# Optimization experiments

Hardware: AMD Instinct MI355X
Metric: run time of the kernel (lower is better)

Reference implementation:

```python
import jax, jax.numpy as jnp
import numpy as np

B, C, VC, H, W = 4, 256, 128, 64, 64


def setup_inputs() -> dict:
    key = jax.random.key(0)
    kx, kq, kk, kv = jax.random.split(key, 4)
    # Conv2d 1x1 no-bias weights are just [out_channels, in_channels] matrices.
    s = 1.0 / np.sqrt(C)
    return {
        "x": jax.random.normal(kx, (B, C, H, W), dtype=jnp.float32),
        "Wq": jax.random.uniform(kq, (VC, C), minval=-s, maxval=s, dtype=jnp.float32),
        "Wk": jax.random.uniform(kk, (VC, C), minval=-s, maxval=s, dtype=jnp.float32),
        "Wv": jax.random.uniform(kv, (VC, C), minval=-s, maxval=s, dtype=jnp.float32),
    }


def reference(x, Wq, Wk, Wv):
    # 1x1 convs == per-pixel channel GEMMs
    Q = jnp.einsum('bchw,dc->bdhw', x, Wq)  # [B, VC, H, W]
    K = jnp.einsum('bchw,dc->bdhw', x, Wk)
    V = jnp.einsum('bchw,dc->bdhw', x, Wv)
    b, d, h, w = Q.shape
    # affinity over all spatial pairs: [B, H, W, H, W]
    aff = jnp.einsum('bdij,bdkl->bijkl', Q, K).reshape(b, h, w, h * w)
    aff = jax.nn.softmax(aff, axis=3).reshape(b, h, w, h, w)
    # attention-weighted aggregation of values
    out = jnp.einsum('bijkl,bdkl->bdij', aff, V)  # [B, VC, H, W]
    return out
```

## Files before the change

### kernel.cpp

```cpp
#include <hip/hip_runtime.h>
#include <hip/hip_bf16.h>

#define B_ 4
#define C_ 256
#define D_ 128
#define N_ 4096

typedef float f32x4 __attribute__((ext_vector_type(4)));
typedef short bf16x8 __attribute__((ext_vector_type(8)));
typedef short s16x4 __attribute__((ext_vector_type(4)));
typedef unsigned short u16;
typedef unsigned int u32;

__device__ __forceinline__ u16 f2bf(float f) {
  unsigned u = __float_as_uint(f);
  u += 0x7fffu + ((u >> 16) & 1u);
  return (u16)(u >> 16);
}
__device__ __forceinline__ float bf2f(u16 v) {
  return __uint_as_float(((u32)v) << 16);
}
__device__ __forceinline__ u32 cvt_pk_bf16(float a, float b) {
  u32 r;
  asm("v_cvt_pk_bf16_f32 %0, %1, %2" : "=v"(r) : "v"(a), "v"(b));
  return r;
}

__global__ __launch_bounds__(256) void castw_kernel(
    const float* __restrict__ Wq, const float* __restrict__ Wk,
    const float* __restrict__ Wv, u16* __restrict__ Whi,
    u16* __restrict__ Wlo) {
  const int i = blockIdx.x * 256 + threadIdx.x;
  const int m = i >> 13;
  const int j = (i & 8191) * 4;
  const float* src = (m == 0) ? Wq : (m == 1) ? Wk : Wv;
  const float scale = (m == 0) ? 1.44269504f : 1.0f;
  const float4 v = *(const float4*)(src + j);
  const float vv[4] = {v.x * scale, v.y * scale, v.z * scale, v.w * scale};
  s16x4 h, l;
#pragma unroll
  for (int k = 0; k < 4; ++k) {
    const u16 hb = f2bf(vv[k]);
    h[k] = (short)hb;
    l[k] = (short)f2bf(vv[k] - bf2f(hb));
  }
  *(s16x4*)&Whi[m * 32768 + j] = h;
  *(s16x4*)&Wlo[m * 32768 + j] = l;
}

__global__ __launch_bounds__(256, 2) void proj_kernel(
    const float* __restrict__ x, const u16* __restrict__ Whi,
    const u16* __restrict__ Wlo, u16* __restrict__ Qo, u16* __restrict__ Ko,
    u16* __restrict__ Vt) {
  __shared__ __align__(16) u16 xs_h[32 * 256];
  __shared__ __align__(16) u16 xs_l[32 * 256];

  const int n0 = blockIdx.x * 32;
  const int b = blockIdx.y;
  const int t = threadIdx.x;
  const int w = t >> 6, lane = t & 63, g = lane >> 4, c = lane & 15;

  {
    const float* xb = x + ((size_t)b * C_) * N_ + n0;
#pragma unroll
    for (int r = 0; r < 8; ++r) {
      const int id = r * 256 + t;
      const int cr = id >> 3, nq = (id & 7) * 4;
      const float4 v = *(const float4*)(xb + (size_t)cr * N_ + nq);
      const float vv[4] = {v.x, v.y, v.z, v.w};
#pragma unroll
      for (int k2 = 0; k2 < 4; ++k2) {
        const int idx2 = (nq + k2) * 256 + (cr ^ (((nq + k2) & 7) << 3));
        const u16 hb = f2bf(vv[k2]);
        xs_h[idx2] = hb;
        xs_l[idx2] = f2bf(vv[k2] - bf2f(hb));
      }
    }
  }
  __syncthreads();

  if (w < 2) {
    const size_t wo = (size_t)w * 32768;
    u16* __restrict__ O = (w == 0 ? Qo : Ko) + (size_t)b * N_ * D_;
#pragma unroll 1
    for (int dt = 0; dt < 8; ++dt) {
      bf16x8 wfh[8], wfl[8];
#pragma unroll
      for (int kc = 0; kc < 8; ++kc) {
        const size_t off = wo + (size_t)(dt * 16 + c) * 256 + kc * 32 + g * 8;
        wfh[kc] = *(const bf16x8*)&Whi[off];
        wfl[kc] = *(const bf16x8*)&Wlo[off];
      }
#pragma unroll
      for (int nt = 0; nt < 2; ++nt) {
        f32x4 a = {0.f, 0.f, 0.f, 0.f};
#pragma unroll
        for (int kc = 0; kc < 8; ++kc) {
          const int xi = (nt * 16 + c) * 256 +
                         ((kc * 32 + g * 8) ^ ((c & 7) << 3));
          const bf16x8 xh = *(const bf16x8*)&xs_h[xi];
          const bf16x8 xl = *(const bf16x8*)&xs_l[xi];
          a = __builtin_amdgcn_mfma_f32_16x16x32_bf16(xh, wfh[kc], a, 0, 0, 0);
          a = __builtin_amdgcn_mfma_f32_16x16x32_bf16(xh, wfl[kc], a, 0, 0, 0);
          a = __builtin_amdgcn_mfma_f32_16x16x32_bf16(xl, wfh[kc], a, 0, 0, 0);
        }
#pragma unroll
        for (int i = 0; i < 4; ++i)
          O[(size_t)(n0 + nt * 16 + g * 4 + i) * D_ + dt * 16 + c] = f2bf(a[i]);
      }
    }
  } else {
    const size_t wo = (size_t)2 * 32768;
    const int d0 = (w - 2) * 64;
    u16* __restrict__ O = Vt + (size_t)b * D_ * N_;
#pragma unroll 1
    for (int dt = 0; dt < 4; ++dt) {
      bf16x8 wfh[8], wfl[8];
#pragma unroll
      for (int kc = 0; kc < 8; ++kc) {
        const size_t off =
            wo + (size_t)(d0 + dt * 16 + c) * 256 + kc * 32 + g * 8;
        wfh[kc] = *(const bf16x8*)&Whi[off];
        wfl[kc] = *(const bf16x8*)&Wlo[off];
      }
#pragma unroll
      for (int nt = 0; nt < 2; ++nt) {
        f32x4 a = {0.f, 0.f, 0.f, 0.f};
#pragma unroll
        for (int kc = 0; kc < 8; ++kc) {
          const int xi = (nt * 16 + c) * 256 +
                         ((kc * 32 + g * 8) ^ ((c & 7) << 3));
          const bf16x8 xh = *(const bf16x8*)&xs_h[xi];
          const bf16x8 xl = *(const bf16x8*)&xs_l[xi];
          a = __builtin_amdgcn_mfma_f32_16x16x32_bf16(wfh[kc], xh, a, 0, 0, 0);
          a = __builtin_amdgcn_mfma_f32_16x16x32_bf16(wfl[kc], xh, a, 0, 0, 0);
          a = __builtin_amdgcn_mfma_f32_16x16x32_bf16(wfh[kc], xl, a, 0, 0, 0);
        }
#pragma unroll
        for (int i = 0; i < 4; ++i)
          O[(size_t)(d0 + dt * 16 + g * 4 + i) * N_ + n0 + nt * 16 + c] =
              f2bf(a[i]);
      }
    }
  }
}

__device__ __forceinline__ int kIdx(int row, int col) {
  return row * 128 + (col ^ ((row & 7) << 3));
}
__device__ __forceinline__ int vIdx(int d, int col) {
  return d * 64 + (col ^ ((d & 7) << 3));
}
__device__ __forceinline__ int pIdx(int q, int col) {
  return q * 64 + (col ^ ((q & 7) << 3));
}

__global__ __launch_bounds__(256, 2) void attn_kernel(
    const u16* __restrict__ Q, const u16* __restrict__ K,
    const u16* __restrict__ Vt, u16* __restrict__ op,
    float* __restrict__ mb, float* __restrict__ lb,
    float* __restrict__ outf, int chunk) {
  __shared__ __align__(16) u16 lds_k[64 * 128];
  __shared__ __align__(16) u16 lds_vt[128 * 64];
  __shared__ __align__(16) u16 lds_p[4][32 * 64];

  const int b = blockIdx.y;
  const int sid = blockIdx.z;
  const int q0 = blockIdx.x * 128;
  const int k0 = sid * chunk;
  const int NT = chunk >> 6;
  const int t = threadIdx.x;
  const int w = t >> 6, lane = t & 63, g = lane >> 4, c = lane & 15;
  const int qw = q0 + w * 32;

  const u16* __restrict__ Qb = Q + (size_t)b * N_ * D_;
  const u16* __restrict__ Kb = K + (size_t)b * N_ * D_;
  const u16* __restrict__ Vb = Vt + (size_t)b * D_ * N_;

  bf16x8 qf[2][4];
#pragma unroll
  for (int qh = 0; qh < 2; ++qh)
#pragma unroll
    for (int kc = 0; kc < 4; ++kc)
      qf[qh][kc] =
          *(const bf16x8*)&Qb[(size_t)(qw + qh * 16 + c) * D_ + kc * 32 + g * 8];

  f32x4 acc[8][2];
#pragma unroll
  for (int dt = 0; dt < 8; ++dt)
#pragma unroll
    for (int qh = 0; qh < 2; ++qh) acc[dt][qh] = (f32x4){0.f, 0.f, 0.f, 0.f};
  float mrow[2] = {-3.0e38f, -3.0e38f};
  float lrow[2] = {0.f, 0.f};
  const float THR = 11.5415603f;

  bf16x8 krg[4], vrg[4];
  auto load_tile = [&](int kbase) {
#pragma unroll
    for (int i = 0; i < 4; ++i) {
      const int idx = i * 256 + t;
      krg[i] = *(const bf16x8*)&Kb[(size_t)(kbase + (idx >> 4)) * D_ + (idx & 15) * 8];
      vrg[i] = *(const bf16x8*)&Vb[(size_t)(idx >> 3) * N_ + kbase + (idx & 7) * 8];
    }
  };
  load_tile(k0);

  u16* __restrict__ pw = lds_p[w];

  for (int kt = 0; kt < NT; ++kt) {
    __syncthreads();
#pragma unroll
    for (int i = 0; i < 4; ++i) {
      const int idx = i * 256 + t;
      *(bf16x8*)&lds_k[kIdx(idx >> 4, (idx & 15) * 8)] = krg[i];
      *(bf16x8*)&lds_vt[vIdx(idx >> 3, (idx & 7) * 8)] = vrg[i];
    }
    if (kt + 1 < NT) load_tile(k0 + (kt + 1) * 64);
    __syncthreads();

    f32x4 s[4][2];
#pragma unroll
    for (int ct = 0; ct < 4; ++ct)
#pragma unroll
      for (int qh = 0; qh < 2; ++qh) s[ct][qh] = (f32x4){0.f, 0.f, 0.f, 0.f};
    __builtin_amdgcn_s_setprio(1);
#pragma unroll
    for (int kc = 0; kc < 4; ++kc) {
#pragma unroll
      for (int ct = 0; ct < 4; ++ct) {
        const bf16x8 kf =
            *(const bf16x8*)&lds_k[kIdx(ct * 16 + c, kc * 32 + g * 8)];
        s[ct][0] = __builtin_amdgcn_mfma_f32_16x16x32_bf16(kf, qf[0][kc], s[ct][0], 0, 0, 0);
        s[ct][1] = __builtin_amdgcn_mfma_f32_16x16x32_bf16(kf, qf[1][kc], s[ct][1], 0, 0, 0);
      }
    }
    __builtin_amdgcn_s_setprio(0);

    float pm[2];
#pragma unroll
    for (int qh = 0; qh < 2; ++qh) {
      const float m0 = fmaxf(fmaxf(s[0][qh][0], s[0][qh][1]),
                             fmaxf(s[0][qh][2], s[0][qh][3]));
      const float m1 = fmaxf(fmaxf(s[1][qh][0], s[1][qh][1]),
                             fmaxf(s[1][qh][2], s[1][qh][3]));
      const float m2 = fmaxf(fmaxf(s[2][qh][0], s[2][qh][1]),
                             fmaxf(s[2][qh][2], s[2][qh][3]));
      const float m3 = fmaxf(fmaxf(s[3][qh][0], s[3][qh][1]),
                             fmaxf(s[3][qh][2], s[3][qh][3]));
      float p = fmaxf(fmaxf(m0, m1), fmaxf(m2, m3));
      p = fmaxf(p, __shfl_xor(p, 16));
      p = fmaxf(p, __shfl_xor(p, 32));
      pm[qh] = p;
    }
    const bool need =
        __any((pm[0] > mrow[0] + THR) || (pm[1] > mrow[1] + THR));
    if (need) {
#pragma unroll
      for (int qh = 0; qh < 2; ++qh) {
        const float mnew = fmaxf(mrow[qh], pm[qh]);
        const float scl = exp2f(mrow[qh] - mnew);
        lrow[qh] *= scl;
        mrow[qh] = mnew;
#pragma unroll
        for (int dt = 0; dt < 8; ++dt) {
          acc[dt][qh][0] *= scl; acc[dt][qh][1] *= scl;
          acc[dt][qh][2] *= scl; acc[dt][qh][3] *= scl;
        }
      }
    }
#pragma unroll
    for (int qh = 0; qh < 2; ++qh) {
      float rs = 0.f;
#pragma unroll
      for (int ct = 0; ct < 4; ++ct)
#pragma unroll
        for (int i = 0; i < 4; ++i) {
          const float p = exp2f(s[ct][qh][i] - mrow[qh]);
          s[ct][qh][i] = p;
          rs += p;
        }
      rs += __shfl_xor(rs, 16);
      rs += __shfl_xor(rs, 32);
      lrow[qh] += rs;
    }

#pragma unroll
    for (int qh = 0; qh < 2; ++qh)
#pragma unroll
      for (int ct = 0; ct < 4; ++ct) {
        const int pi = pIdx(qh * 16 + c, ct * 16 + g * 4);
        union { u32 w2[2]; s16x4 v; } pu;
        pu.w2[0] = cvt_pk_bf16(s[ct][qh][0], s[ct][qh][1]);
        pu.w2[1] = cvt_pk_bf16(s[ct][qh][2], s[ct][qh][3]);
        *(s16x4*)&pw[pi] = pu.v;
      }
    asm volatile("" ::: "memory");

    __builtin_amdgcn_s_setprio(1);
#pragma unroll
    for (int kc = 0; kc < 2; ++kc) {
      const bf16x8 pf0 = *(const bf16x8*)&pw[pIdx(c, kc * 32 + g * 8)];
      const bf16x8 pf1 = *(const bf16x8*)&pw[pIdx(16 + c, kc * 32 + g * 8)];
#pragma unroll
      for (int dt = 0; dt < 8; ++dt) {
        const bf16x8 vf =
            *(const bf16x8*)&lds_vt[vIdx(dt * 16 + c, kc * 32 + g * 8)];
        acc[dt][0] = __builtin_amdgcn_mfma_f32_16x16x32_bf16(vf, pf0, acc[dt][0], 0, 0, 0);
        acc[dt][1] = __builtin_amdgcn_mfma_f32_16x16x32_bf16(vf, pf1, acc[dt][1], 0, 0, 0);
      }
    }
    __builtin_amdgcn_s_setprio(0);
  }

#pragma unroll
  for (int qh = 0; qh < 2; ++qh) {
    const int n = qw + qh * 16 + c;
    if (mb) {
      u16* __restrict__ ob = op + ((size_t)(sid * B_ + b) * D_) * N_;
#pragma unroll
      for (int dt = 0; dt < 8; ++dt)
#pragma unroll
        for (int i = 0; i < 4; ++i)
          ob[(size_t)(dt * 16 + g * 4 + i) * N_ + n] = f2bf(acc[dt][qh][i]);
      if (g == 0) {
        mb[(size_t)(sid * B_ + b) * N_ + n] = mrow[qh];
        lb[(size_t)(sid * B_ + b) * N_ + n] = lrow[qh];
      }
    } else {
      const float linv = 1.0f / lrow[qh];
      float* __restrict__ ob = outf + (size_t)b * D_ * N_;
#pragma unroll
      for (int dt = 0; dt < 8; ++dt)
#pragma unroll
        for (int i = 0; i < 4; ++i)
          ob[(size_t)(dt * 16 + g * 4 + i) * N_ + n] = acc[dt][qh][i] * linv;
    }
  }
}

__global__ __launch_bounds__(256) void combine_kernel(
    const u16* __restrict__ op, const float* __restrict__ mbu,
    const float* __restrict__ lbu, float* __restrict__ out, int S) {
  const int idx = blockIdx.x * 256 + threadIdx.x;
  const int n0 = (idx & (N_ / 4 - 1)) * 4;
  const int bd = idx >> 10;
  const int b = bd >> 7, d = bd & (D_ - 1);

  float4 msv[8], lsv[8];
  float M0 = -3e38f, M1 = -3e38f, M2 = -3e38f, M3 = -3e38f;
#pragma unroll
  for (int s = 0; s < 8; ++s)
    if (s < S) {
      msv[s] = *(const float4*)&mbu[(size_t)(s * B_ + b) * N_ + n0];
      lsv[s] = *(const float4*)&lbu[(size_t)(s * B_ + b) * N_ + n0];
      M0 = fmaxf(M0, msv[s].x); M1 = fmaxf(M1, msv[s].y);
      M2 = fmaxf(M2, msv[s].z); M3 = fmaxf(M3, msv[s].w);
    }
  float d0 = 0.f, d1 = 0.f, d2 = 0.f, d3 = 0.f;
  float a0 = 0.f, a1 = 0.f, a2 = 0.f, a3 = 0.f;
#pragma unroll
  for (int s = 0; s < 8; ++s)
    if (s < S) {
      const float w0 = exp2f(msv[s].x - M0);
      const float w1 = exp2f(msv[s].y - M1);
      const float w2 = exp2f(msv[s].z - M2);
      const float w3 = exp2f(msv[s].w - M3);
      d0 += lsv[s].x * w0; d1 += lsv[s].y * w1;
      d2 += lsv[s].z * w2; d3 += lsv[s].w * w3;
      const s16x4 o =
          *(const s16x4*)&op[((size_t)(s * B_ + b) * D_ + d) * N_ + n0];
      a0 += w0 * bf2f((u16)o[0]); a1 += w1 * bf2f((u16)o[1]);
      a2 += w2 * bf2f((u16)o[2]); a3 += w3 * bf2f((u16)o[3]);
    }
  float4 r = {a0 / d0, a1 / d1, a2 / d2, a3 / d3};
  *(float4*)&out[((size_t)b * D_ + d) * N_ + n0] = r;
}

extern "C" void kernel_launch(void* const* d_in, const int* in_sizes, int n_in,
                              void* d_out, int out_size, void* d_ws, size_t ws_size,
                              hipStream_t stream) {
  const float* x  = (const float*)d_in[0];
  const float* Wq = (const float*)d_in[1];
  const float* Wk = (const float*)d_in[2];
  const float* Wv = (const float*)d_in[3];
  float* out = (float*)d_out;

  u16* whi  = (u16*)d_ws;
  u16* wlo  = whi + (size_t)3 * 128 * 256;
  u16* q_ws = wlo + (size_t)3 * 128 * 256;
  u16* k_ws = q_ws + (size_t)B_ * N_ * D_;
  u16* v_ws = k_ws + (size_t)B_ * N_ * D_;

  castw_kernel<<<96, 256, 0, stream>>>(Wq, Wk, Wv, whi, wlo);
  proj_kernel<<<dim3(N_ / 32, B_), 256, 0, stream>>>(x, whi, wlo, q_ws, k_ws,
                                                     v_ws);

  const size_t baseB =
      ((size_t)6 * 128 * 256 + (size_t)3 * B_ * N_ * D_) * 2;
  int S = 0;
  for (int cand = 8; cand >= 1; cand >>= 1) {
    const size_t need = baseB + (size_t)cand * ((size_t)B_ * D_ * N_ * 2 +
                                                (size_t)2 * B_ * N_ * 4);
    if (ws_size >= need) { S = cand; break; }
  }
  if (S > 0) {
    u16* opb = (u16*)((char*)d_ws + baseB);
    float* mbuf = (float*)(opb + (size_t)S * B_ * D_ * N_);
    float* lbuf = mbuf + (size_t)S * B_ * N_;
    attn_kernel<<<dim3(N_ / 128, B_, S), 256, 0, stream>>>(
        q_ws, k_ws, v_ws, opb, mbuf, lbuf, nullptr, N_ / S);
    combine_kernel<<<(B_ * D_ * N_ / 4) / 256, 256, 0, stream>>>(opb, mbuf,
                                                                 lbuf, out, S);
  } else {
    attn_kernel<<<dim3(N_ / 128, B_, 1), 256, 0, stream>>>(
        q_ws, k_ws, v_ws, nullptr, nullptr, nullptr, out, N_);
  }
}
```

Measured before the change: 102.8 us.

## Load K fragments directly from global memory instead of staging through LDS

Drops the LDS staging buffer for K. Each wave now reads its K fragments straight from global memory (likely L2-resident), double-buffered across the kc steps, while only V still goes through LDS. The barrier after the LDS store moves to just before the PV MFMAs, so the QK^T phase can overlap with other waves. In exchange, the four waves of a block each issue redundant global K loads, and the QK MFMAs become exposed to global-memory latency.

```diff
diff --git a/kernel.cpp b/kernel.cpp
--- a/kernel.cpp
+++ b/kernel.cpp
@@ -145,9 +145,6 @@
   }
 }
 
-__device__ __forceinline__ int kIdx(int row, int col) {
-  return row * 128 + (col ^ ((row & 7) << 3));
-}
 __device__ __forceinline__ int vIdx(int d, int col) {
   return d * 64 + (col ^ ((d & 7) << 3));
 }
@@ -160,7 +157,6 @@
     const u16* __restrict__ Vt, u16* __restrict__ op,
     float* __restrict__ mb, float* __restrict__ lb,
     float* __restrict__ outf, int chunk) {
-  __shared__ __align__(16) u16 lds_k[64 * 128];
   __shared__ __align__(16) u16 lds_vt[128 * 64];
   __shared__ __align__(16) u16 lds_p[4][32 * 64];
 
@@ -194,16 +190,15 @@
   float lrow[2] = {0.f, 0.f};
   const float THR = 11.5415603f;
 
-  bf16x8 krg[4], vrg[4];
-  auto load_tile = [&](int kbase) {
+  bf16x8 vrg[4];
+  auto load_v = [&](int kbase) {
 #pragma unroll
     for (int i = 0; i < 4; ++i) {
       const int idx = i * 256 + t;
-      krg[i] = *(const bf16x8*)&Kb[(size_t)(kbase + (idx >> 4)) * D_ + (idx & 15) * 8];
       vrg[i] = *(const bf16x8*)&Vb[(size_t)(idx >> 3) * N_ + kbase + (idx & 7) * 8];
     }
   };
-  load_tile(k0);
+  load_v(k0);
 
   u16* __restrict__ pw = lds_p[w];
 
@@ -212,29 +207,39 @@
 #pragma unroll
     for (int i = 0; i < 4; ++i) {
       const int idx = i * 256 + t;
-      *(bf16x8*)&lds_k[kIdx(idx >> 4, (idx & 15) * 8)] = krg[i];
       *(bf16x8*)&lds_vt[vIdx(idx >> 3, (idx & 7) * 8)] = vrg[i];
     }
-    if (kt + 1 < NT) load_tile(k0 + (kt + 1) * 64);
-    __syncthreads();
-
+    if (kt + 1 < NT) load_v(k0 + (kt + 1) * 64);
+
+    const u16* __restrict__ Kt = Kb + (size_t)(k0 + kt * 64) * D_;
     f32x4 s[4][2];
 #pragma unroll
     for (int ct = 0; ct < 4; ++ct)
 #pragma unroll
       for (int qh = 0; qh < 2; ++qh) s[ct][qh] = (f32x4){0.f, 0.f, 0.f, 0.f};
-    __builtin_amdgcn_s_setprio(1);
+
+    bf16x8 ka[4], kb2[4];
+#pragma unroll
+    for (int ct = 0; ct < 4; ++ct)
+      ka[ct] = *(const bf16x8*)&Kt[(size_t)(ct * 16 + c) * D_ + g * 8];
 #pragma unroll
     for (int kc = 0; kc < 4; ++kc) {
+      const bf16x8* cur = (kc & 1) ? kb2 : ka;
+      bf16x8* nxt = (kc & 1) ? ka : kb2;
+      if (kc < 3) {
+#pragma unroll
+        for (int ct = 0; ct < 4; ++ct)
+          nxt[ct] = *(const bf16x8*)&Kt[(size_t)(ct * 16 + c) * D_ +
+                                        (kc + 1) * 32 + g * 8];
+      }
+      __builtin_amdgcn_s_setprio(1);
 #pragma unroll
       for (int ct = 0; ct < 4; ++ct) {
-        const bf16x8 kf =
-            *(const bf16x8*)&lds_k[kIdx(ct * 16 + c, kc * 32 + g * 8)];
-        s[ct][0] = __builtin_amdgcn_mfma_f32_16x16x32_bf16(kf, qf[0][kc], s[ct][0], 0, 0, 0);
-        s[ct][1] = __builtin_amdgcn_mfma_f32_16x16x32_bf16(kf, qf[1][kc], s[ct][1], 0, 0, 0);
-      }
-    }
-    __builtin_amdgcn_s_setprio(0);
+        s[ct][0] = __builtin_amdgcn_mfma_f32_16x16x32_bf16(cur[ct], qf[0][kc], s[ct][0], 0, 0, 0);
+        s[ct][1] = __builtin_amdgcn_mfma_f32_16x16x32_bf16(cur[ct], qf[1][kc], s[ct][1], 0, 0, 0);
+      }
+      __builtin_amdgcn_s_setprio(0);
+    }
 
     float pm[2];
 #pragma unroll
@@ -296,6 +301,8 @@
       }
     asm volatile("" ::: "memory");
 
+    __syncthreads();
+
     __builtin_amdgcn_s_setprio(1);
 #pragma unroll
     for (int kc = 0; kc < 2; ++kc) {
```

After: 134.6 us. 1.31x slower.
